# Kernel tuning notes

Measured on AMD Instinct MI355X. Metric: run time of the kernel, lower is better.

The kernel has to match this reference:

```python
import jax, jax.numpy as jnp
import numpy as np
from jax import lax

B, CIN, COUT, H, W, K = 8, 256, 256, 64, 64, 3
KK = K * K
PAD, STRIDE = 1, 1
EPS = 1e-5


def setup_inputs() -> dict:
    key = jax.random.key(0)
    k0, k1, k2 = jax.random.split(key, 3)
    x = jax.random.normal(k0, (B, CIN, H, W), jnp.float32)
    # offset/mask predicting conv: 3*K*K output channels (o1, o2, mask)
    w_off = jax.random.normal(k1, (3 * KK, CIN, K, K), jnp.float32) * 0.01
    b_off = jnp.zeros((3 * KK,), jnp.float32)
    # main deformable conv weight
    weight = jax.random.normal(k2, (COUT, CIN, K, K), jnp.float32) / np.sqrt(CIN * KK).astype(np.float32)
    bias = jnp.zeros((COUT,), jnp.float32)
    gamma = jnp.ones((COUT,), jnp.float32)
    beta = jnp.zeros((COUT,), jnp.float32)
    return {"x": x, "w_off": w_off, "b_off": b_off, "weight": weight,
            "bias": bias, "gamma": gamma, "beta": beta}


def _bilinear_sample(img, ph, pw):
    """img: [C,H,W]; ph,pw: [KK,H,W] float sample positions. Zero outside. -> [C,KK,H,W]"""
    h0 = jnp.floor(ph).astype(jnp.int32)
    w0 = jnp.floor(pw).astype(jnp.int32)
    h1, w1 = h0 + 1, w0 + 1
    lh = ph - h0.astype(ph.dtype)
    lw = pw - w0.astype(pw.dtype)
    hh, hw = 1.0 - lh, 1.0 - lw

    def corner(hi, wi):
        valid = (hi >= 0) & (hi < H) & (wi >= 0) & (wi < W)
        hc = jnp.clip(hi, 0, H - 1)
        wc = jnp.clip(wi, 0, W - 1)
        v = img[:, hc, wc]  # [C,KK,H,W]
        return v * valid.astype(img.dtype)[None]

    return (corner(h0, w0) * (hh * hw)[None] + corner(h0, w1) * (hh * lw)[None]
            + corner(h1, w0) * (lh * hw)[None] + corner(h1, w1) * (lh * lw)[None])


def _forward(x, w_off, b_off, weight, bias, gamma, beta):
    dn = ('NCHW', 'OIHW', 'NCHW')
    # offset/mask branch (standard conv)
    om = lax.conv_general_dilated(x, w_off, (STRIDE, STRIDE), ((PAD, PAD), (PAD, PAD)),
                                  dimension_numbers=dn) + b_off[None, :, None, None]
    o1, o2, m = jnp.split(om, 3, axis=1)
    offset = jnp.concatenate([o1, o2], axis=1)          # [B, 2*KK, H, W]
    off_h = offset[:, 0::2]                             # [B, KK, H, W] dy per tap
    off_w = offset[:, 1::2]                             # [B, KK, H, W] dx per tap
    mask = jax.nn.sigmoid(m)                            # [B, KK, H, W]

    taps = jnp.arange(KK)
    base_h = (taps // K - PAD).astype(jnp.float32)[:, None, None] \
        + (jnp.arange(H, dtype=jnp.float32) * STRIDE)[None, :, None]  # [KK,H,1]
    base_w = (taps % K - PAD).astype(jnp.float32)[:, None, None] \
        + (jnp.arange(W, dtype=jnp.float32) * STRIDE)[None, None, :]  # [KK,1,W]
    ph = base_h[None] + off_h                           # [B,KK,H,W]
    pw = base_w[None] + off_w

    sampled = jax.vmap(_bilinear_sample)(x, ph, pw)     # [B,CIN,KK,H,W]
    sampled = sampled * mask[:, None]                   # modulated (DCNv2)

    y = jnp.einsum('bckhw,ock->bohw', sampled, weight.reshape(COUT, CIN, KK))
    y = y + bias[None, :, None, None]

    # BatchNorm2d (training mode: batch statistics) + ReLU
    mean = y.mean(axis=(0, 2, 3))
    var = y.var(axis=(0, 2, 3))
    yn = (y - mean[None, :, None, None]) * lax.rsqrt(var + EPS)[None, :, None, None]
    out = jax.nn.relu(gamma[None, :, None, None] * yn + beta[None, :, None, None])
    return out


def reference(x, w_off, b_off, weight, bias, gamma, beta):
    return _forward(x, w_off, b_off, weight, bias, gamma, beta)
```

## Files before the change

### kernel.cpp

```cpp
#include <hip/hip_runtime.h>
#include <cstdint>

#define BB    8
#define CIN   256
#define COUT  256
#define HH    64
#define WW    64

typedef __attribute__((ext_vector_type(8))) short    s16x8;
typedef __attribute__((ext_vector_type(8))) unsigned short u16x8;
typedef __attribute__((ext_vector_type(4))) unsigned short u16x4;
typedef __attribute__((ext_vector_type(4))) float    f32x4;

__device__ __forceinline__ float bf2f(unsigned short u) {
    unsigned int v = ((unsigned int)u) << 16;
    return __builtin_bit_cast(float, v);
}
__device__ __forceinline__ unsigned short f2bf(float f) {
    unsigned int u = __builtin_bit_cast(unsigned int, f);
    unsigned int r = (u + 0x7FFFu + ((u >> 16) & 1u)) >> 16;
    return (unsigned short)r;
}
__device__ __forceinline__ unsigned short f2bf_rz(float f) {
    return (unsigned short)(__builtin_bit_cast(unsigned int, f) >> 16);
}

__global__ void k_pack(const float* __restrict__ x,
                       const float* __restrict__ w,
                       const float* __restrict__ woff,
                       unsigned short* __restrict__ xT,
                       unsigned short* __restrict__ wTk,
                       unsigned short* __restrict__ wofT,
                       float* __restrict__ gsum,
                       float* __restrict__ gssq) {
    int blk = blockIdx.x;
    int t = threadIdx.x;
    __shared__ float tile[64 * 65];
    if (blk == 0 && t < 256) { gsum[t] = 0.f; gssq[t] = 0.f; }
    if (blk < 2048) {
        int b    = blk & 7;
        int rest = blk >> 3;
        int h    = rest >> 2;
        int c0   = (rest & 3) * 64;
#pragma unroll
        for (int r = 0; r < 16; ++r) {
            int idx = t + r * 256;
            int i = idx >> 6, w_ = idx & 63;
            tile[i * 65 + w_] = x[(((b * 256 + c0 + i) * 64 + h) * 64) + w_];
        }
        __syncthreads();
#pragma unroll
        for (int r = 0; r < 2; ++r) {
            int idx = t + r * 256;
            int w_ = idx >> 3;
            int c8 = (idx & 7) * 8;
            u16x8 res;
#pragma unroll
            for (int k = 0; k < 8; ++k) res[k] = f2bf(tile[(c8 + k) * 65 + w_]);
            *reinterpret_cast<u16x8*>(&xT[((b * 64 + h) * 64 + w_) * 256 + c0 + c8]) = res;
        }
    } else if (blk < 4352) {
        int idx = (blk - 2048) * 256 + t;
        int j   = idx & 7;
        int q   = (idx >> 3) & 3;
        int o16 = (idx >> 5) & 15;
        int n16 = (idx >> 9) & 15;
        int kc  = (idx >> 13) & 7;
        int tp  = idx >> 16;
        int c = kc * 32 + q * 8 + j;
        int o = n16 * 16 + o16;
        wTk[idx] = f2bf(w[(o * 256 + c) * 9 + tp]);
    } else {
        int idx = (blk - 4352) * 256 + t;
        int c  = idx & 255;
        int j  = (idx >> 8) & 31;
        int tp = idx >> 13;
        wofT[idx] = f2bf((j < 27) ? woff[(j * 256 + c) * 9 + tp] : 0.f);
    }
}

__global__ __launch_bounds__(512, 4)
void k_main(const unsigned short* __restrict__ xT,
            const unsigned short* __restrict__ wTk,
            const unsigned short* __restrict__ wofT,
            const float* __restrict__ boffg,
            const float* __restrict__ bias,
            unsigned short* __restrict__ y16,
            float* __restrict__ gsum, float* __restrict__ gssq) {
    __shared__ __align__(16) char smem[76032];
    int blk = blockIdx.x;
    int b = blk & 7, h = blk >> 3;
    int pblk = b * 64 + h;
    int t = threadIdx.x;
    int lane = t & 63, wv = t >> 6;
    int lm = lane & 15, q = lane >> 4;
    const f32x4 FZ = {0.f, 0.f, 0.f, 0.f};

    {
        unsigned short* S3 = (unsigned short*)smem;
        float* PART = (float*)(smem + 53856);
        float* OMS  = (float*)(smem + 67584);
        f32x4 oacc0 = FZ, oacc1 = FZ;
        int myTile = wv & 3;
        int myKH   = wv >> 2;
        int p0w = myTile * 16;
        for (int cc = 0; cc < 2; ++cc) {
            __syncthreads();
            if (t < 96) {
                int rr = t >> 5, col = (t >> 4) & 1, c8 = (t & 15) * 8;
                u16x8 z = {0,0,0,0,0,0,0,0};
                *reinterpret_cast<u16x8*>(&S3[(rr * 66 + col * 65) * 136 + c8]) = z;
            }
#pragma unroll
            for (int r = 0; r < 6; ++r) {
                int v = t + r * 512;
                int rr = v >> 10, rem = v & 1023;
                int w_ = rem >> 4, c8 = (rem & 15) * 8;
                int hr = h + rr - 1;
                u16x8 d = {0,0,0,0,0,0,0,0};
                if (hr >= 0 && hr < 64)
                    d = *reinterpret_cast<const u16x8*>(xT + ((b * 64 + hr) * 64 + w_) * 256 + cc * 128 + c8);
                *reinterpret_cast<u16x8*>(&S3[(rr * 66 + w_ + 1) * 136 + c8]) = d;
            }
            __syncthreads();
            {
                int boff = cc * 128 + myKH * 64 + q * 8;
                s16x8 pb[4], nb[4];
                {
                    const unsigned short* wb = wofT + (0 * 32 + lm) * 256 + boff;
                    pb[0] = *reinterpret_cast<const s16x8*>(wb);
                    pb[1] = *reinterpret_cast<const s16x8*>(wb + 32);
                    pb[2] = *reinterpret_cast<const s16x8*>(wb + 16 * 256);
                    pb[3] = *reinterpret_cast<const s16x8*>(wb + 16 * 256 + 32);
                }
#pragma unroll
                for (int tp = 0; tp < 9; ++tp) {
                    if (tp < 8) {
                        const unsigned short* wb = wofT + ((tp + 1) * 32 + lm) * 256 + boff;
                        nb[0] = *reinterpret_cast<const s16x8*>(wb);
                        nb[1] = *reinterpret_cast<const s16x8*>(wb + 32);
                        nb[2] = *reinterpret_cast<const s16x8*>(wb + 16 * 256);
                        nb[3] = *reinterpret_cast<const s16x8*>(wb + 16 * 256 + 32);
                    }
                    int dh = tp / 3, dw_ = tp % 3;
                    int arow = (dh * 66 + p0w + lm + dw_) * 136 + myKH * 64 + q * 8;
                    s16x8 a0 = *reinterpret_cast<const s16x8*>(&S3[arow]);
                    s16x8 a1 = *reinterpret_cast<const s16x8*>(&S3[arow + 32]);
                    oacc0 = __builtin_amdgcn_mfma_f32_16x16x32_bf16(a0, pb[0], oacc0, 0, 0, 0);
                    oacc0 = __builtin_amdgcn_mfma_f32_16x16x32_bf16(a1, pb[1], oacc0, 0, 0, 0);
                    oacc1 = __builtin_amdgcn_mfma_f32_16x16x32_bf16(a0, pb[2], oacc1, 0, 0, 0);
                    oacc1 = __builtin_amdgcn_mfma_f32_16x16x32_bf16(a1, pb[3], oacc1, 0, 0, 0);
#pragma unroll
                    for (int i = 0; i < 4; ++i) pb[i] = nb[i];
                }
            }
        }
        __syncthreads();
        if (wv >= 4) {
#pragma unroll
            for (int i = 0; i < 4; ++i) {
                int prow = p0w + q * 4 + i;
                PART[prow * 33 + lm]      = oacc0[i];
                PART[prow * 33 + 16 + lm] = oacc1[i];
            }
        }
        __syncthreads();
        if (wv < 4) {
#pragma unroll
            for (int n = 0; n < 2; ++n) {
                int j = n * 16 + lm;
                float bj = (j < 27) ? boffg[j] : 0.f;
                f32x4 a = n ? oacc1 : oacc0;
#pragma unroll
                for (int i = 0; i < 4; ++i) {
                    int prow = p0w + q * 4 + i;
                    OMS[prow * 33 + j] = a[i] + PART[prow * 33 + j] + bj;
                }
            }
        }
        __syncthreads();
    }

    unsigned short* S = (unsigned short*)smem;
    float* OMS = (float*)(smem + 67584);
    f32x4 acc[4][4];
#pragma unroll
    for (int m = 0; m < 4; ++m)
#pragma unroll
        for (int n = 0; n < 4; ++n) acc[m][n] = FZ;

    if (wv >= 4) {
        int pw = wv - 4;
        int s  = lane & 7;
        int pA = pw * 16 + (lane >> 3);
        int pB = pA + 8;
        int rb = b * 4096;

        float wgA[4], wgB[4];
        int   adA[4], adB[4];

        auto setup = [&](int tp, int p, float* wgt, int* ad) {
            float oh = OMS[p * 33 + 2 * tp];
            float ow = OMS[p * 33 + 2 * tp + 1];
            float mv = OMS[p * 33 + 18 + tp];
            float mk = 1.f / (1.f + __expf(-mv));
            float ph = (float)(h + tp / 3 - 1) + oh;
            float pw_ = (float)(p + tp % 3 - 1) + ow;
            float fh0 = floorf(ph), fw0 = floorf(pw_);
            int ih0 = (int)fh0, iw0 = (int)fw0;
            float lh = ph - fh0, lw = pw_ - fw0;
            float hh = 1.f - lh, hw_ = 1.f - lw;
            bool vh0 = (ih0 >= 0) & (ih0 < 64);
            bool vh1 = (ih0 + 1 >= 0) & (ih0 + 1 < 64);
            bool vw0 = (iw0 >= 0) & (iw0 < 64);
            bool vw1 = (iw0 + 1 >= 0) & (iw0 + 1 < 64);
            wgt[0] = hh * hw_ * mk * (float)(vh0 & vw0);
            wgt[1] = hh * lw  * mk * (float)(vh0 & vw1);
            wgt[2] = lh * hw_ * mk * (float)(vh1 & vw0);
            wgt[3] = lh * lw  * mk * (float)(vh1 & vw1);
            int ch0 = min(max(ih0, 0), 63), ch1 = min(max(ih0 + 1, 0), 63);
            int cw0 = min(max(iw0, 0), 63), cw1 = min(max(iw0 + 1, 0), 63);
            ad[0] = ((rb + ch0 * 64 + cw0) * 256);
            ad[1] = ((rb + ch0 * 64 + cw1) * 256);
            ad[2] = ((rb + ch1 * 64 + cw0) * 256);
            ad[3] = ((rb + ch1 * 64 + cw1) * 256);
        };

        u16x8 rP[4], rQ[4];
        auto issueSet = [&](const int* ad, int j, u16x8* r) {
            int off = j * 64 + s * 8;
#pragma unroll
            for (int c = 0; c < 4; ++c)
                r[c] = *reinterpret_cast<const u16x8*>(xT + ad[c] + off);
        };
        auto blendSet = [&](int buf, int p, const float* wgt, int j, u16x8* r) {
            u16x8 res;
#pragma unroll
            for (int k = 0; k < 8; ++k) {
                float v = wgt[0] * bf2f(r[0][k]);
                v = fmaf(wgt[1], bf2f(r[1][k]), v);
                v = fmaf(wgt[2], bf2f(r[2][k]), v);
                v = fmaf(wgt[3], bf2f(r[3][k]), v);
                res[k] = f2bf_rz(v);
            }
            *reinterpret_cast<u16x8*>(&S[buf * 16896 + p * 264 + j * 64 + s * 8]) = res;
        };
        auto fillTap = [&](int tp, int buf) {
            setup(tp, pA, wgA, adA);
            setup(tp, pB, wgB, adB);
            issueSet(adA, 0, rP);
            issueSet(adA, 1, rQ);
            blendSet(buf, pA, wgA, 0, rP);  issueSet(adA, 2, rP);
            blendSet(buf, pA, wgA, 1, rQ);  issueSet(adA, 3, rQ);
            blendSet(buf, pA, wgA, 2, rP);  issueSet(adB, 0, rP);
            blendSet(buf, pA, wgA, 3, rQ);  issueSet(adB, 1, rQ);
            blendSet(buf, pB, wgB, 0, rP);  issueSet(adB, 2, rP);
            blendSet(buf, pB, wgB, 1, rQ);  issueSet(adB, 3, rQ);
            blendSet(buf, pB, wgB, 2, rP);
            blendSet(buf, pB, wgB, 3, rQ);
        };

        fillTap(0, 0);
        __syncthreads();
        for (int tp = 0; tp < 9; ++tp) {
            if (tp < 8) fillTap(tp + 1, (tp + 1) & 1);
            __syncthreads();
        }
    } else {
        __syncthreads();
        for (int tp = 0; tp < 9; ++tp) {
            const unsigned short* Sc = &S[(tp & 1) * 16896];
            const unsigned short* wtap = wTk + (size_t)tp * 65536
                                       + (size_t)(wv * 4) * 512 + lm * 32 + q * 8;
            s16x8 wbuf[2][4];
#pragma unroll
            for (int n = 0; n < 4; ++n)
                wbuf[0][n] = *reinterpret_cast<const s16x8*>(wtap + n * 512);
#pragma unroll
            for (int kc = 0; kc < 8; ++kc) {
                if (kc < 7) {
                    const unsigned short* wb = wtap + (kc + 1) * 8192;
#pragma unroll
                    for (int n = 0; n < 4; ++n)
                        wbuf[(kc + 1) & 1][n] = *reinterpret_cast<const s16x8*>(wb + n * 512);
                }
#pragma unroll
                for (int mt = 0; mt < 4; ++mt) {
                    s16x8 a = *reinterpret_cast<const s16x8*>(
                        &Sc[(mt * 16 + lm) * 264 + kc * 32 + q * 8]);
#pragma unroll
                    for (int n = 0; n < 4; ++n)
                        acc[mt][n] = __builtin_amdgcn_mfma_f32_16x16x32_bf16(
                            a, wbuf[kc & 1][n], acc[mt][n], 0, 0, 0);
                }
            }
            __syncthreads();
        }
    }

    unsigned short* T = (unsigned short*)smem;
    if (wv < 4) {
#pragma unroll
        for (int nt = 0; nt < 4; ++nt) {
            int o = wv * 64 + nt * 16 + lm;
            float bo = bias[o];
            float sacc = 0.f, ssacc = 0.f;
#pragma unroll
            for (int mt = 0; mt < 4; ++mt) {
#pragma unroll
                for (int i = 0; i < 4; ++i) {
                    float v = acc[mt][nt][i] + bo;
                    T[o * 68 + mt * 16 + q * 4 + i] = f2bf(v);
                    sacc += v; ssacc += v * v;
                }
            }
            sacc  += __shfl_xor(sacc, 16);
            sacc  += __shfl_xor(sacc, 32);
            ssacc += __shfl_xor(ssacc, 16);
            ssacc += __shfl_xor(ssacc, 32);
            if (q == 0) {
                atomicAdd(&gsum[o], sacc);
                atomicAdd(&gssq[o], ssacc);
            }
        }
    }
    __syncthreads();
    u16x4* yv = reinterpret_cast<u16x4*>(y16) + (size_t)pblk * 4096;
#pragma unroll
    for (int k = 0; k < 8; ++k) {
        int u = t + k * 512;
        int o = u >> 4, g2 = u & 15;
        yv[o * 16 + g2] = *reinterpret_cast<const u16x4*>(&T[o * 68 + g2 * 4]);
    }
}

__global__ void k_bnrelu(const unsigned short* __restrict__ y16,
                         const float* __restrict__ gsum, const float* __restrict__ gssq,
                         const float* __restrict__ gamma, const float* __restrict__ beta,
                         float* __restrict__ out) {
    int i = blockIdx.x;
    int t = threadIdx.x;
    int b    = i & 7;
    int rest = i >> 3;
    int h    = rest & 63;
    int o0   = (rest >> 6) * 64;
    int pblk = b * 64 + h;
    __shared__ float sc[64], sh[64];
    if (t < 64) {
        int o = o0 + t;
        const float invn = 1.f / 32768.f;
        float mean = gsum[o] * invn;
        float var = gssq[o] * invn - mean * mean;
        float inv = rsqrtf(var + 1e-5f);
        float s = gamma[o] * inv;
        sc[t] = s;
        sh[t] = beta[o] - mean * s;
    }
    __syncthreads();
    const u16x8* yv = reinterpret_cast<const u16x8*>(
        y16 + ((size_t)pblk * 256 + o0) * 64);
    float* obase = out + ((size_t)b * 256 + o0) * 4096 + h * 64;
#pragma unroll
    for (int r = 0; r < 2; ++r) {
        int c = t + r * 256;
        int row = c >> 3, g = c & 7;
        u16x8 d = yv[row * 8 + g];
        float scl = sc[row], shf = sh[row];
        float4 v0, v1;
        v0.x = fmaxf(bf2f(d[0]) * scl + shf, 0.f);
        v0.y = fmaxf(bf2f(d[1]) * scl + shf, 0.f);
        v0.z = fmaxf(bf2f(d[2]) * scl + shf, 0.f);
        v0.w = fmaxf(bf2f(d[3]) * scl + shf, 0.f);
        v1.x = fmaxf(bf2f(d[4]) * scl + shf, 0.f);
        v1.y = fmaxf(bf2f(d[5]) * scl + shf, 0.f);
        v1.z = fmaxf(bf2f(d[6]) * scl + shf, 0.f);
        v1.w = fmaxf(bf2f(d[7]) * scl + shf, 0.f);
        float* op = obase + row * 4096 + g * 8;
        *reinterpret_cast<float4*>(op)     = v0;
        *reinterpret_cast<float4*>(op + 4) = v1;
    }
}

extern "C" void kernel_launch(void* const* d_in, const int* in_sizes, int n_in,
                              void* d_out, int out_size, void* d_ws, size_t ws_size,
                              hipStream_t stream) {
    const float* x      = (const float*)d_in[0];
    const float* w_off  = (const float*)d_in[1];
    const float* b_off  = (const float*)d_in[2];
    const float* weight = (const float*)d_in[3];
    const float* bias   = (const float*)d_in[4];
    const float* gamma  = (const float*)d_in[5];
    const float* beta   = (const float*)d_in[6];

    char* ws = (char*)d_ws;
    const size_t OFF_XT    = 0;
    const size_t OFF_WT    = OFF_XT + 16777216;
    const size_t OFF_WOFT  = OFF_WT + 1179648;
    const size_t OFF_Y16   = OFF_WOFT + 147456;
    const size_t OFF_SUM   = OFF_Y16 + 16777216;
    const size_t OFF_SUMSQ = OFF_SUM + 1024;

    unsigned short* xT   = (unsigned short*)(ws + OFF_XT);
    unsigned short* wTk  = (unsigned short*)(ws + OFF_WT);
    unsigned short* wofT = (unsigned short*)(ws + OFF_WOFT);
    unsigned short* y16  = (unsigned short*)(ws + OFF_Y16);
    float* gsum  = (float*)(ws + OFF_SUM);
    float* gssq  = (float*)(ws + OFF_SUMSQ);

    k_pack  <<<4640, 256, 0, stream>>>(x, weight, w_off, xT, wTk, wofT, gsum, gssq);
    k_main  <<< 512, 512, 0, stream>>>(xT, wTk, wofT, b_off, bias, y16, gsum, gssq);
    k_bnrelu<<<2048, 256, 0, stream>>>(y16, gsum, gssq, gamma, beta, (float*)d_out);
}
```

Measured before the change: 202.2 us.

## Process two output rows per block to reuse weight fragments across rows

Each k_main block now computes two adjacent output rows instead of one, with half as many blocks. Each weight fragment loaded for the main MFMA loop is applied to both rows' sampled tiles, halving weight reads per output. The offset conv is re-split so each wave covers the full input-channel range for one row tile, which removes the cross-wave partial-sum reduction through shared memory. In exchange, LDS use doubles to about 152KB, accumulator registers double, the launch bound drops to 2, and gather waves must build twice as many sampled tiles per tap, so fewer waves per CU are left to hide gather latency.

```diff
diff --git a/kernel.cpp b/kernel.cpp
--- a/kernel.cpp
+++ b/kernel.cpp
@@ -79,7 +79,7 @@
     }
 }
 
-__global__ __launch_bounds__(512, 4)
+__global__ __launch_bounds__(512, 2)
 void k_main(const unsigned short* __restrict__ xT,
             const unsigned short* __restrict__ wTk,
             const unsigned short* __restrict__ wofT,
@@ -87,36 +87,35 @@
             const float* __restrict__ bias,
             unsigned short* __restrict__ y16,
             float* __restrict__ gsum, float* __restrict__ gssq) {
-    __shared__ __align__(16) char smem[76032];
+    __shared__ __align__(16) char smem[152064];
     int blk = blockIdx.x;
-    int b = blk & 7, h = blk >> 3;
-    int pblk = b * 64 + h;
+    int b = blk & 7, hp = blk >> 3;
+    int h0 = hp * 2;
+    int pblk0 = b * 64 + h0;
     int t = threadIdx.x;
     int lane = t & 63, wv = t >> 6;
     int lm = lane & 15, q = lane >> 4;
     const f32x4 FZ = {0.f, 0.f, 0.f, 0.f};
+    float* OMS = (float*)(smem + 135168);
 
     {
         unsigned short* S3 = (unsigned short*)smem;
-        float* PART = (float*)(smem + 53856);
-        float* OMS  = (float*)(smem + 67584);
         f32x4 oacc0 = FZ, oacc1 = FZ;
-        int myTile = wv & 3;
-        int myKH   = wv >> 2;
-        int p0w = myTile * 16;
+        int p0w   = (wv & 3) * 16;
+        int hbase = wv >> 2;
         for (int cc = 0; cc < 2; ++cc) {
             __syncthreads();
-            if (t < 96) {
+            if (t < 128) {
                 int rr = t >> 5, col = (t >> 4) & 1, c8 = (t & 15) * 8;
                 u16x8 z = {0,0,0,0,0,0,0,0};
                 *reinterpret_cast<u16x8*>(&S3[(rr * 66 + col * 65) * 136 + c8]) = z;
             }
 #pragma unroll
-            for (int r = 0; r < 6; ++r) {
+            for (int r = 0; r < 8; ++r) {
                 int v = t + r * 512;
                 int rr = v >> 10, rem = v & 1023;
                 int w_ = rem >> 4, c8 = (rem & 15) * 8;
-                int hr = h + rr - 1;
+                int hr = h0 - 1 + rr;
                 u16x8 d = {0,0,0,0,0,0,0,0};
                 if (hr >= 0 && hr < 64)
                     d = *reinterpret_cast<const u16x8*>(xT + ((b * 64 + hr) * 64 + w_) * 256 + cc * 128 + c8);
@@ -124,68 +123,58 @@
             }
             __syncthreads();
             {
-                int boff = cc * 128 + myKH * 64 + q * 8;
-                s16x8 pb[4], nb[4];
+                int boff = cc * 128 + q * 8;
+                s16x8 pb[8], nb[8];
                 {
-                    const unsigned short* wb = wofT + (0 * 32 + lm) * 256 + boff;
-                    pb[0] = *reinterpret_cast<const s16x8*>(wb);
-                    pb[1] = *reinterpret_cast<const s16x8*>(wb + 32);
-                    pb[2] = *reinterpret_cast<const s16x8*>(wb + 16 * 256);
-                    pb[3] = *reinterpret_cast<const s16x8*>(wb + 16 * 256 + 32);
+                    const unsigned short* wb = wofT + lm * 256 + boff;
+#pragma unroll
+                    for (int kc = 0; kc < 4; ++kc) {
+                        pb[kc]     = *reinterpret_cast<const s16x8*>(wb + kc * 32);
+                        pb[4 + kc] = *reinterpret_cast<const s16x8*>(wb + 4096 + kc * 32);
+                    }
                 }
 #pragma unroll
                 for (int tp = 0; tp < 9; ++tp) {
                     if (tp < 8) {
                         const unsigned short* wb = wofT + ((tp + 1) * 32 + lm) * 256 + boff;
-                        nb[0] = *reinterpret_cast<const s16x8*>(wb);
-                        nb[1] = *reinterpret_cast<const s16x8*>(wb + 32);
-                        nb[2] = *reinterpret_cast<const s16x8*>(wb + 16 * 256);
-                        nb[3] = *reinterpret_cast<const s16x8*>(wb + 16 * 256 + 32);
+#pragma unroll
+                        for (int kc = 0; kc < 4; ++kc) {
+                            nb[kc]     = *reinterpret_cast<const s16x8*>(wb + kc * 32);
+                            nb[4 + kc] = *reinterpret_cast<const s16x8*>(wb + 4096 + kc * 32);
+                        }
                     }
                     int dh = tp / 3, dw_ = tp % 3;
-                    int arow = (dh * 66 + p0w + lm + dw_) * 136 + myKH * 64 + q * 8;
-                    s16x8 a0 = *reinterpret_cast<const s16x8*>(&S3[arow]);
-                    s16x8 a1 = *reinterpret_cast<const s16x8*>(&S3[arow + 32]);
-                    oacc0 = __builtin_amdgcn_mfma_f32_16x16x32_bf16(a0, pb[0], oacc0, 0, 0, 0);
-                    oacc0 = __builtin_amdgcn_mfma_f32_16x16x32_bf16(a1, pb[1], oacc0, 0, 0, 0);
-                    oacc1 = __builtin_amdgcn_mfma_f32_16x16x32_bf16(a0, pb[2], oacc1, 0, 0, 0);
-                    oacc1 = __builtin_amdgcn_mfma_f32_16x16x32_bf16(a1, pb[3], oacc1, 0, 0, 0);
-#pragma unroll
-                    for (int i = 0; i < 4; ++i) pb[i] = nb[i];
+                    int arow = ((dh + hbase) * 66 + p0w + lm + dw_) * 136 + q * 8;
+#pragma unroll
+                    for (int kc = 0; kc < 4; ++kc) {
+                        s16x8 a = *reinterpret_cast<const s16x8*>(&S3[arow + kc * 32]);
+                        oacc0 = __builtin_amdgcn_mfma_f32_16x16x32_bf16(a, pb[kc],     oacc0, 0, 0, 0);
+                        oacc1 = __builtin_amdgcn_mfma_f32_16x16x32_bf16(a, pb[4 + kc], oacc1, 0, 0, 0);
+                    }
+#pragma unroll
+                    for (int i = 0; i < 8; ++i) pb[i] = nb[i];
                 }
             }
         }
         __syncthreads();
-        if (wv >= 4) {
+#pragma unroll
+        for (int n = 0; n < 2; ++n) {
+            int j = n * 16 + lm;
+            float bj = (j < 27) ? boffg[j] : 0.f;
+            f32x4 a = n ? oacc1 : oacc0;
 #pragma unroll
             for (int i = 0; i < 4; ++i) {
-                int prow = p0w + q * 4 + i;
-                PART[prow * 33 + lm]      = oacc0[i];
-                PART[prow * 33 + 16 + lm] = oacc1[i];
-            }
-        }
-        __syncthreads();
-        if (wv < 4) {
-#pragma unroll
-            for (int n = 0; n < 2; ++n) {
-                int j = n * 16 + lm;
-                float bj = (j < 27) ? boffg[j] : 0.f;
-                f32x4 a = n ? oacc1 : oacc0;
-#pragma unroll
-                for (int i = 0; i < 4; ++i) {
-                    int prow = p0w + q * 4 + i;
-                    OMS[prow * 33 + j] = a[i] + PART[prow * 33 + j] + bj;
-                }
+                int pg = hbase * 64 + p0w + q * 4 + i;
+                OMS[pg * 33 + j] = a[i] + bj;
             }
         }
         __syncthreads();
     }
 
     unsigned short* S = (unsigned short*)smem;
-    float* OMS = (float*)(smem + 67584);
-    f32x4 acc[4][4];
-#pragma unroll
-    for (int m = 0; m < 4; ++m)
+    f32x4 acc[8][4];
+#pragma unroll
+    for (int m = 0; m < 8; ++m)
 #pragma unroll
         for (int n = 0; n < 4; ++n) acc[m][n] = FZ;
 
@@ -196,15 +185,16 @@
         int pB = pA + 8;
         int rb = b * 4096;
 
-        float wgA[4], wgB[4];
-        int   adA[4], adB[4];
-
-        auto setup = [&](int tp, int p, float* wgt, int* ad) {
-            float oh = OMS[p * 33 + 2 * tp];
-            float ow = OMS[p * 33 + 2 * tp + 1];
-            float mv = OMS[p * 33 + 18 + tp];
+        float wgA[4], wgB[4], wgC[4], wgD[4];
+        int   adA[4], adB[4], adC[4], adD[4];
+
+        auto setup = [&](int tp, int tile, int p, float* wgt, int* ad) {
+            int pg = tile * 64 + p;
+            float oh = OMS[pg * 33 + 2 * tp];
+            float ow = OMS[pg * 33 + 2 * tp + 1];
+            float mv = OMS[pg * 33 + 18 + tp];
             float mk = 1.f / (1.f + __expf(-mv));
-            float ph = (float)(h + tp / 3 - 1) + oh;
+            float ph = (float)(h0 + tile + tp / 3 - 1) + oh;
             float pw_ = (float)(p + tp % 3 - 1) + ow;
             float fh0 = floorf(ph), fw0 = floorf(pw_);
             int ih0 = (int)fh0, iw0 = (int)fw0;
@@ -233,7 +223,7 @@
             for (int c = 0; c < 4; ++c)
                 r[c] = *reinterpret_cast<const u16x8*>(xT + ad[c] + off);
         };
-        auto blendSet = [&](int buf, int p, const float* wgt, int j, u16x8* r) {
+        auto blendSet = [&](int tile, int buf, int p, const float* wgt, int j, u16x8* r) {
             u16x8 res;
 #pragma unroll
             for (int k = 0; k < 8; ++k) {
@@ -243,21 +233,31 @@
                 v = fmaf(wgt[3], bf2f(r[3][k]), v);
                 res[k] = f2bf_rz(v);
             }
-            *reinterpret_cast<u16x8*>(&S[buf * 16896 + p * 264 + j * 64 + s * 8]) = res;
+            *reinterpret_cast<u16x8*>(
+                &S[((tile << 1) | buf) * 16896 + p * 264 + j * 64 + s * 8]) = res;
         };
         auto fillTap = [&](int tp, int buf) {
-            setup(tp, pA, wgA, adA);
-            setup(tp, pB, wgB, adB);
-            issueSet(adA, 0, rP);
-            issueSet(adA, 1, rQ);
-            blendSet(buf, pA, wgA, 0, rP);  issueSet(adA, 2, rP);
-            blendSet(buf, pA, wgA, 1, rQ);  issueSet(adA, 3, rQ);
-            blendSet(buf, pA, wgA, 2, rP);  issueSet(adB, 0, rP);
-            blendSet(buf, pA, wgA, 3, rQ);  issueSet(adB, 1, rQ);
-            blendSet(buf, pB, wgB, 0, rP);  issueSet(adB, 2, rP);
-            blendSet(buf, pB, wgB, 1, rQ);  issueSet(adB, 3, rQ);
-            blendSet(buf, pB, wgB, 2, rP);
-            blendSet(buf, pB, wgB, 3, rQ);
+            setup(tp, 0, pA, wgA, adA);
+            setup(tp, 0, pB, wgB, adB);
+            setup(tp, 1, pA, wgC, adC);
+            setup(tp, 1, pB, wgD, adD);
+            issueSet(adA, 0, rP);              issueSet(adA, 1, rQ);
+            blendSet(0, buf, pA, wgA, 0, rP);  issueSet(adA, 2, rP);
+            blendSet(0, buf, pA, wgA, 1, rQ);  issueSet(adA, 3, rQ);
+            blendSet(0, buf, pA, wgA, 2, rP);  issueSet(adB, 0, rP);
+            blendSet(0, buf, pA, wgA, 3, rQ);  issueSet(adB, 1, rQ);
+            blendSet(0, buf, pB, wgB, 0, rP);  issueSet(adB, 2, rP);
+            blendSet(0, buf, pB, wgB, 1, rQ);  issueSet(adB, 3, rQ);
+            blendSet(0, buf, pB, wgB, 2, rP);  issueSet(adC, 0, rP);
+            blendSet(0, buf, pB, wgB, 3, rQ);  issueSet(adC, 1, rQ);
+            blendSet(1, buf, pA, wgC, 0, rP);  issueSet(adC, 2, rP);
+            blendSet(1, buf, pA, wgC, 1, rQ);  issueSet(adC, 3, rQ);
+            blendSet(1, buf, pA, wgC, 2, rP);  issueSet(adD, 0, rP);
+            blendSet(1, buf, pA, wgC, 3, rQ);  issueSet(adD, 1, rQ);
+            blendSet(1, buf, pB, wgD, 0, rP);  issueSet(adD, 2, rP);
+            blendSet(1, buf, pB, wgD, 1, rQ);  issueSet(adD, 3, rQ);
+            blendSet(1, buf, pB, wgD, 2, rP);
+            blendSet(1, buf, pB, wgD, 3, rQ);
         };
 
         fillTap(0, 0);
@@ -269,7 +269,9 @@
     } else {
         __syncthreads();
         for (int tp = 0; tp < 9; ++tp) {
-            const unsigned short* Sc = &S[(tp & 1) * 16896];
+            int cur = tp & 1;
+            const unsigned short* Sc0 = &S[cur * 16896];
+            const unsigned short* Sc1 = &S[(2 | cur) * 16896];
             const unsigned short* wtap = wTk + (size_t)tp * 65536
                                        + (size_t)(wv * 4) * 512 + lm * 32 + q * 8;
             s16x8 wbuf[2][4];
@@ -286,12 +288,17 @@
                 }
 #pragma unroll
                 for (int mt = 0; mt < 4; ++mt) {
-                    s16x8 a = *reinterpret_cast<const s16x8*>(
-                        &Sc[(mt * 16 + lm) * 264 + kc * 32 + q * 8]);
-#pragma unroll
-                    for (int n = 0; n < 4; ++n)
-                        acc[mt][n] = __builtin_amdgcn_mfma_f32_16x16x32_bf16(
-                            a, wbuf[kc & 1][n], acc[mt][n], 0, 0, 0);
+                    s16x8 a0 = *reinterpret_cast<const s16x8*>(
+                        &Sc0[(mt * 16 + lm) * 264 + kc * 32 + q * 8]);
+                    s16x8 a1 = *reinterpret_cast<const s16x8*>(
+                        &Sc1[(mt * 16 + lm) * 264 + kc * 32 + q * 8]);
+#pragma unroll
+                    for (int n = 0; n < 4; ++n) {
+                        acc[mt][n]     = __builtin_amdgcn_mfma_f32_16x16x32_bf16(
+                            a0, wbuf[kc & 1][n], acc[mt][n], 0, 0, 0);
+                        acc[4 + mt][n] = __builtin_amdgcn_mfma_f32_16x16x32_bf16(
+                            a1, wbuf[kc & 1][n], acc[4 + mt][n], 0, 0, 0);
+                    }
                 }
             }
             __syncthreads();
@@ -299,38 +306,49 @@
     }
 
     unsigned short* T = (unsigned short*)smem;
+    float sacc[4] = {0.f, 0.f, 0.f, 0.f};
+    float ssacc[4] = {0.f, 0.f, 0.f, 0.f};
+    for (int tile = 0; tile < 2; ++tile) {
+        __syncthreads();
+        if (wv < 4) {
+#pragma unroll
+            for (int nt = 0; nt < 4; ++nt) {
+                int o = wv * 64 + nt * 16 + lm;
+                float bo = bias[o];
+#pragma unroll
+                for (int mt = 0; mt < 4; ++mt) {
+#pragma unroll
+                    for (int i = 0; i < 4; ++i) {
+                        float v = acc[tile * 4 + mt][nt][i] + bo;
+                        T[o * 68 + mt * 16 + q * 4 + i] = f2bf(v);
+                        sacc[nt] += v; ssacc[nt] += v * v;
+                    }
+                }
+            }
+        }
+        __syncthreads();
+        u16x4* yv = reinterpret_cast<u16x4*>(y16) + (size_t)(pblk0 + tile) * 4096;
+#pragma unroll
+        for (int k = 0; k < 8; ++k) {
+            int u = t + k * 512;
+            int o = u >> 4, g2 = u & 15;
+            yv[o * 16 + g2] = *reinterpret_cast<const u16x4*>(&T[o * 68 + g2 * 4]);
+        }
+    }
     if (wv < 4) {
 #pragma unroll
         for (int nt = 0; nt < 4; ++nt) {
             int o = wv * 64 + nt * 16 + lm;
-            float bo = bias[o];
-            float sacc = 0.f, ssacc = 0.f;
-#pragma unroll
-            for (int mt = 0; mt < 4; ++mt) {
-#pragma unroll
-                for (int i = 0; i < 4; ++i) {
-                    float v = acc[mt][nt][i] + bo;
-                    T[o * 68 + mt * 16 + q * 4 + i] = f2bf(v);
-                    sacc += v; ssacc += v * v;
-                }
-            }
-            sacc  += __shfl_xor(sacc, 16);
-            sacc  += __shfl_xor(sacc, 32);
-            ssacc += __shfl_xor(ssacc, 16);
-            ssacc += __shfl_xor(ssacc, 32);
+            float sa = sacc[nt], ss = ssacc[nt];
+            sa += __shfl_xor(sa, 16);
+            sa += __shfl_xor(sa, 32);
+            ss += __shfl_xor(ss, 16);
+            ss += __shfl_xor(ss, 32);
             if (q == 0) {
-                atomicAdd(&gsum[o], sacc);
-                atomicAdd(&gssq[o], ssacc);
-            }
-        }
-    }
-    __syncthreads();
-    u16x4* yv = reinterpret_cast<u16x4*>(y16) + (size_t)pblk * 4096;
-#pragma unroll
-    for (int k = 0; k < 8; ++k) {
-        int u = t + k * 512;
-        int o = u >> 4, g2 = u & 15;
-        yv[o * 16 + g2] = *reinterpret_cast<const u16x4*>(&T[o * 68 + g2 * 4]);
+                atomicAdd(&gsum[o], sa);
+                atomicAdd(&gssq[o], ss);
+            }
+        }
     }
 }
 
@@ -408,6 +426,6 @@
     float* gssq  = (float*)(ws + OFF_SUMSQ);
 
     k_pack  <<<4640, 256, 0, stream>>>(x, weight, w_off, xT, wTk, wofT, gsum, gssq);
-    k_main  <<< 512, 512, 0, stream>>>(xT, wTk, wofT, b_off, bias, y16, gsum, gssq);
+    k_main  <<< 256, 512, 0, stream>>>(xT, wTk, wofT, b_off, bias, y16, gsum, gssq);
     k_bnrelu<<<2048, 256, 0, stream>>>(y16, gsum, gssq, gamma, beta, (float*)d_out);
 }
```

Measured after the change: 206.9 us. +2.3%, slower.
